# Kernel tuning notes

Hardware: AMD Instinct MI355X
Metric: run time of the kernel (lower is better)

The kernel has to match this reference:

```python
import jax, jax.numpy as jnp
import numpy as np

D_MODEL = 1024
D_STATE = 64
N_HEADS = 16
CHUNK = 64


def segsum(x):
    # x: (..., T) -> (..., T, T) with [i, j] = sum_{j<k<=i} x[k], -inf above diagonal
    T = x.shape[-1]
    xx = jnp.broadcast_to(x[..., None], x.shape + (T,))  # [i, j] = x[i]
    lower = jnp.tril(jnp.ones((T, T), dtype=bool), -1)
    xs = jnp.cumsum(jnp.where(lower, xx, 0.0), axis=-2)
    keep = jnp.tril(jnp.ones((T, T), dtype=bool), 0)
    return jnp.where(keep, xs, -jnp.inf)


def ssd_minimal(X, A, B, C, block_len):
    b, L, h, p = X.shape
    n = B.shape[-1]
    c = L // block_len
    l = block_len
    X = X.reshape(b, c, l, h, p)
    A = A.reshape(b, c, l, h).transpose(0, 3, 1, 2)  # b h c l
    B = B.reshape(b, c, l, h, n)
    C = C.reshape(b, c, l, h, n)
    A_cumsum = jnp.cumsum(A, axis=-1)  # b h c l
    Lmat = jnp.exp(segsum(A))  # b h c l l
    Y_diag = jnp.einsum('bclhn,bcshn,bhcls,bcshp->bclhp', C, B, Lmat, X)
    decay_states = jnp.exp(A_cumsum[:, :, :, -1:] - A_cumsum)  # b h c l
    states = jnp.einsum('bclhn,bhcl,bclhp->bchpn', B, decay_states, X)
    init = jnp.zeros_like(states[:, :1])
    states = jnp.concatenate([init, states], axis=1)  # b (c+1) h p n
    A_last = A_cumsum[:, :, :, -1]  # b h c
    decay_chunk = jnp.exp(segsum(jnp.pad(A_last, ((0, 0), (0, 0), (1, 0)))))  # b h (c+1) (c+1)
    new_states = jnp.einsum('bhzc,bchpn->bzhpn', decay_chunk, states)
    states, final_state = new_states[:, :-1], new_states[:, -1]
    state_decay_out = jnp.exp(A_cumsum)  # b h c l
    Y_off = jnp.einsum('bclhn,bchpn,bhcl->bclhp', C, states, state_decay_out)
    Y = (Y_diag + Y_off).reshape(b, L, h, p)
    return Y, final_state


def mamba2_forward(x, W_in, W_dt, b_dt, W_B, W_C, W_out, A_log):
    b, L, d = x.shape
    h, n = N_HEADS, D_STATE
    p = d // h
    # seqlen divisible by CHUNK -> no padding needed (pad_len == 0)
    xz = x @ W_in.T  # (b, L, 2d)
    x_in, z = xz[..., :d], xz[..., d:]
    dt = jax.nn.softplus(x @ W_dt.T + b_dt)  # (b, L, h)
    A = -jnp.exp(A_log)[None, None, :] * dt  # (b, L, h)
    B = (x @ W_B.T).reshape(b, L, h, n)
    C = (x @ W_C.T).reshape(b, L, h, n)
    X = x_in.reshape(b, L, h, p) * dt[..., None]
    Y, new_state = ssd_minimal(X, A, B, C, CHUNK)
    y = Y.reshape(b, L, d) * jax.nn.silu(z)
    y = y @ W_out.T
    return y, new_state


def setup_inputs() -> dict:
    key = jax.random.key(0)
    ks = jax.random.split(key, 7)
    d, h, n = D_MODEL, N_HEADS, D_STATE
    x = jax.random.normal(ks[0], (2, 4096, d), dtype=jnp.float32)
    # xavier_uniform with gain 0.5 for in/out proj
    lim_in = 0.5 * np.sqrt(6.0 / (d + 2 * d))
    W_in = jax.random.uniform(ks[1], (2 * d, d), minval=-lim_in, maxval=lim_in, dtype=jnp.float32)
    lim_out = 0.5 * np.sqrt(6.0 / (d + d))
    W_out = jax.random.uniform(ks[2], (d, d), minval=-lim_out, maxval=lim_out, dtype=jnp.float32)
    # default torch Linear init (kaiming-uniform-ish): U(-1/sqrt(fan_in), 1/sqrt(fan_in))
    lim = 1.0 / np.sqrt(d)
    W_dt = jax.random.uniform(ks[3], (h, d), minval=-lim, maxval=lim, dtype=jnp.float32)
    b_dt = jnp.zeros((h,), dtype=jnp.float32)
    W_B = jax.random.uniform(ks[4], (h * n, d), minval=-lim, maxval=lim, dtype=jnp.float32)
    W_C = jax.random.uniform(ks[5], (h * n, d), minval=-lim, maxval=lim, dtype=jnp.float32)
    A_log = jnp.log(jnp.linspace(1.0, 16.0, h)).astype(jnp.float32)
    return {"x": x, "W_in": W_in, "W_dt": W_dt, "b_dt": b_dt, "W_B": W_B, "W_C": W_C, "W_out": W_out, "A_log": A_log}


def reference(x, W_in, W_dt, b_dt, W_B, W_C, W_out, A_log):
    return mamba2_forward(x, W_in, W_dt, b_dt, W_B, W_C, W_out, A_log)
```

## Files before the change

### kernel.cpp

```cpp
#include <hip/hip_runtime.h>
#include <cstdint>
#include <cstddef>

#define NTOK 8192

typedef __bf16 bf16x8 __attribute__((ext_vector_type(8)));
typedef float f32x4 __attribute__((ext_vector_type(4)));
typedef float f32x4v __attribute__((ext_vector_type(4)));
typedef unsigned short u16x8 __attribute__((ext_vector_type(8)));

__device__ __forceinline__ float b2f(unsigned short u) {
    return __uint_as_float(((unsigned int)u) << 16);
}
__device__ __forceinline__ unsigned short f2b(float f) {
    unsigned int u = __float_as_uint(f);
    u += 0x7FFFu + ((u >> 16) & 1u);
    return (unsigned short)(u >> 16);
}

__device__ __forceinline__ void async_lds16(unsigned short* lds, const unsigned short* g) {
    __builtin_amdgcn_global_load_lds(
        (const __attribute__((address_space(1))) unsigned int*)g,
        (__attribute__((address_space(3))) unsigned int*)lds,
        16, 0, 0);
}

__global__ __launch_bounds__(256) void prep(
    const float* __restrict__ x, const float* __restrict__ W_in,
    const float* __restrict__ W_B, const float* __restrict__ W_C,
    unsigned short* __restrict__ xb, unsigned short* __restrict__ Wst,
    const float* __restrict__ s16a, const float* __restrict__ s16b,
    float* __restrict__ alogf, float* __restrict__ bdtf)
{
    const long i = (long)blockIdx.x * 256 + threadIdx.x;
    const float* src; unsigned short* dst; long off;
    if (i < 1048576)      { src = x;    dst = xb;            off = i; }
    else if (i < 1310720) { src = W_in; dst = Wst;           off = i - 1048576; }
    else if (i < 1441792) { src = W_B;  dst = Wst + 2097152; off = i - 1310720; }
    else if (i < 1572864) { src = W_C;  dst = Wst + 3145728; off = i - 1441792; }
    else {
        if (i == 1572864) {
            float ma = 0.f, mb = 0.f;
            for (int k = 0; k < 16; k++) { ma = fmaxf(ma, fabsf(s16a[k])); mb = fmaxf(mb, fabsf(s16b[k])); }
            const float* alog = (ma >= mb) ? s16a : s16b;
            const float* bdt  = (ma >= mb) ? s16b : s16a;
            for (int k = 0; k < 16; k++) { alogf[k] = alog[k]; bdtf[k] = bdt[k]; }
        }
        return;
    }
    const f32x4v* p = (const f32x4v*)(src + off * 8);
    f32x4v a = p[0], b = p[1];
    u16x8 v;
#pragma unroll
    for (int t = 0; t < 4; t++) { v[t] = f2b(a[t]); v[t + 4] = f2b(b[t]); }
    *(u16x8*)(dst + off * 8) = v;
}

__global__ __launch_bounds__(256) void f32_to_bf16(
    const float* __restrict__ in, unsigned short* __restrict__ out, int n8)
{
    const int i = blockIdx.x * 256 + threadIdx.x;
    if (i >= n8) return;
    const f32x4v* p = (const f32x4v*)(in + (long)i * 8);
    f32x4v a = p[0], b = p[1];
    u16x8 v;
#pragma unroll
    for (int t = 0; t < 4; t++) { v[t] = f2b(a[t]); v[t + 4] = f2b(b[t]); }
    *(u16x8*)(out + (long)i * 8) = v;
}

__global__ __launch_bounds__(256) void dt_kernel(
    const float* __restrict__ x, const float* __restrict__ Wdt,
    const float* __restrict__ bdt, const float* __restrict__ Alog,
    float* __restrict__ dtp, float* __restrict__ Ap)
{
    const int token = blockIdx.x * 16 + (threadIdx.x >> 4);
    const int h = threadIdx.x & 15;
    const f32x4v* xr = (const f32x4v*)(x + (long)token * 1024);
    const f32x4v* wr = (const f32x4v*)(Wdt + h * 1024);
    float s0 = bdt[h], s1 = 0.f;
#pragma unroll 8
    for (int k = 0; k < 256; k += 2) {
        f32x4v a0 = xr[k], w0 = wr[k];
        f32x4v a1 = xr[k + 1], w1 = wr[k + 1];
        s0 += a0[0] * w0[0] + a0[1] * w0[1] + a0[2] * w0[2] + a0[3] * w0[3];
        s1 += a1[0] * w1[0] + a1[1] * w1[1] + a1[2] * w1[2] + a1[3] * w1[3];
    }
    const float s = s0 + s1;
    const float dtv = (s > 15.f) ? s : log1pf(expf(s));
    dtp[token * 16 + h] = dtv;
    Ap[token * 16 + h] = -expf(Alog[h]) * dtv;
}

template <int MODE, int NI>
__global__ __launch_bounds__(512, 2) void gemm256(
    const unsigned short* __restrict__ A, const unsigned short* __restrict__ W,
    const int NT_N, const int N, const int K,
    void* __restrict__ out0, unsigned short* __restrict__ out1,
    unsigned short* __restrict__ out2, unsigned short* __restrict__ out3,
    const float* __restrict__ dtp)
{
    constexpr int BN = NI * 64;

    __shared__ unsigned short As[2][256 * 64];
    __shared__ unsigned short Ws[2][BN * 64];

    const int tid = threadIdx.x;
    const int lane = tid & 63;
    const int warp = tid >> 6;
    const int wm = warp >> 2;
    const int wn = warp & 3;
    const int qm = lane & 15;
    const int quad = lane >> 4;

    const int nwg = gridDim.x;
    const int cpx = nwg >> 3;
    const int bid = blockIdx.x;
    const int swz = (bid & 7) * cpx + (bid >> 3);
    const int bx = swz % NT_N;
    const int by = swz / NT_N;
    const long arow0 = (long)by * 256;
    const long wrow0 = (long)bx * BN;

    const int srow = tid >> 3;
    const int sgc = ((tid & 7) ^ (srow & 7)) * 8;

    f32x4 acc[8][NI];
    const f32x4 zero = {0.f, 0.f, 0.f, 0.f};
#pragma unroll
    for (int i = 0; i < 8; i++)
#pragma unroll
        for (int j = 0; j < NI; j++) acc[i][j] = zero;

    auto stage = [&](int buf, int k0) {
#pragma unroll
        for (int r = 0; r < 4; r++)
            async_lds16(As[buf] + r * 4096 + tid * 8,
                        A + (arow0 + r * 64 + srow) * (long)K + k0 + sgc);
#pragma unroll
        for (int r = 0; r < NI; r++)
            async_lds16(Ws[buf] + r * 4096 + tid * 8,
                        W + (wrow0 + r * 64 + srow) * (long)K + k0 + sgc);
    };
    const int rx = (qm & 7) << 3;
    auto compute = [&](const unsigned short* Ab, const unsigned short* Wb) {
#pragma unroll
        for (int kk = 0; kk < 64; kk += 32) {
            bf16x8 fa[8], fb[NI];
#pragma unroll
            for (int mi = 0; mi < 8; mi++) {
                const int row = wm * 128 + mi * 16 + qm;
                fa[mi] = *(const bf16x8*)(Ab + ((row * 64 + kk + quad * 8) ^ rx));
            }
#pragma unroll
            for (int ni = 0; ni < NI; ni++) {
                const int row = wn * (NI * 16) + ni * 16 + qm;
                fb[ni] = *(const bf16x8*)(Wb + ((row * 64 + kk + quad * 8) ^ rx));
            }
#pragma unroll
            for (int mi = 0; mi < 8; mi++)
#pragma unroll
                for (int ni = 0; ni < NI; ni++)
                    acc[mi][ni] = __builtin_amdgcn_mfma_f32_16x16x32_bf16(
                        fa[mi], fb[ni], acc[mi][ni], 0, 0, 0);
        }
    };

    const int nk = K >> 6;
    int cur = 0;
    stage(0, 0);
    __syncthreads();
    for (int t = 1; t < nk; t++) {
        stage(cur ^ 1, t << 6);
        compute(As[cur], Ws[cur]);
        __syncthreads();
        cur ^= 1;
    }
    compute(As[cur], Ws[cur]);

#pragma unroll
    for (int mi = 0; mi < 8; mi++)
#pragma unroll
        for (int ni = 0; ni < NI; ni++)
#pragma unroll
            for (int r = 0; r < 4; r++) {
                const long row = arow0 + wm * 128 + mi * 16 + quad * 4 + r;
                const int col = (int)wrow0 + wn * (NI * 16) + ni * 16 + qm;
                const float v = acc[mi][ni][r];
                if (MODE == 0) {
                    ((float*)out0)[row * N + col] = v;
                } else {
                    const int seg = col >> 10, cc = col & 1023;
                    if (seg == 0) {
                        ((unsigned short*)out0)[row * 1024 + cc] = f2b(v * dtp[row * 16 + (cc >> 6)]);
                    } else if (seg == 1) {
                        out1[row * 1024 + cc] = f2b(v / (1.f + expf(-v)));
                    } else if (seg == 2) {
                        out2[row * 1024 + cc] = f2b(v);
                    } else {
                        out3[row * 1024 + cc] = f2b(v);
                    }
                }
            }
}

__global__ __launch_bounds__(256) void ssd_states(
    const unsigned short* __restrict__ Xb, const unsigned short* __restrict__ Bb,
    const float* __restrict__ Ap, float* __restrict__ st_out,
    float* __restrict__ Alast)
{
    __shared__ __align__(16) unsigned short Xh[64 * 64];
    __shared__ __align__(16) unsigned short Xl[64 * 64];
    __shared__ __align__(16) unsigned short Bt[64 * 64];
    __shared__ float dec[64];

    const int blk = blockIdx.x;
    const int h = blk & 15;
    const int c = (blk >> 4) & 63;
    const int b = blk >> 10;
    const long tokenbase = (long)b * 4096 + (long)c * 64;
    const int tid = threadIdx.x;
    const int lane = tid & 63;
    const int w = tid >> 6;
    const int qm = lane & 15;
    const int quad = lane >> 4;

    const int row = tid & 63;
    u16x8 rx[2], rb[2];
#pragma unroll
    for (int i = 0; i < 2; i++) {
        const int ch = (tid >> 6) + 4 * i;
        const long g = (tokenbase + row) * 1024 + h * 64 + ch * 8;
        rx[i] = *(const u16x8*)(Xb + g);
        rb[i] = *(const u16x8*)(Bb + g);
    }
    if (tid < 64) {
        float v = Ap[(tokenbase + tid) * 16 + h];
#pragma unroll
        for (int off = 1; off < 64; off <<= 1) {
            const float u = __shfl_up(v, off, 64);
            if (tid >= off) v += u;
        }
        const float tot = __shfl(v, 63, 64);
        dec[tid] = expf(tot - v);
        if (tid == 63) Alast[(b * 16 + h) * 64 + c] = v;
    }
    __syncthreads();

    const float dv = dec[row];
#pragma unroll
    for (int i = 0; i < 2; i++) {
        const int ch = (tid >> 6) + 4 * i;
#pragma unroll
        for (int t = 0; t < 8; t++) {
            const int pn = ch * 8 + t;
            const int d = (pn * 64 + row) ^ (t << 3);
            const float xd = b2f(rx[i][t]) * dv;
            const unsigned short hi = f2b(xd);
            Xh[d] = hi;
            Xl[d] = f2b(xd - b2f(hi));
            Bt[d] = rb[i][t];
        }
    }
    __syncthreads();

    f32x4 acc[4];
    const f32x4 zero = {0.f, 0.f, 0.f, 0.f};
#pragma unroll
    for (int ni = 0; ni < 4; ni++) acc[ni] = zero;
#pragma unroll
    for (int kk2 = 0; kk2 < 2; kk2++) {
        const int ko = kk2 * 32 + quad * 8;
        const int ra = 16 * w + qm;
        const int da = (ra * 64 + ko) ^ ((ra & 7) << 3);
        bf16x8 fxh = *(const bf16x8*)(Xh + da);
        bf16x8 fxl = *(const bf16x8*)(Xl + da);
#pragma unroll
        for (int ni = 0; ni < 4; ni++) {
            const int rn = ni * 16 + qm;
            bf16x8 fb = *(const bf16x8*)(Bt + ((rn * 64 + ko) ^ ((rn & 7) << 3)));
            acc[ni] = __builtin_amdgcn_mfma_f32_16x16x32_bf16(fxh, fb, acc[ni], 0, 0, 0);
            acc[ni] = __builtin_amdgcn_mfma_f32_16x16x32_bf16(fxl, fb, acc[ni], 0, 0, 0);
        }
    }
    const long sbase = (long)blk * 4096;
    const int p0 = 16 * w + quad * 4;
#pragma unroll
    for (int ni = 0; ni < 4; ni++)
#pragma unroll
        for (int r = 0; r < 4; r++)
            st_out[sbase + (p0 + r) * 64 + ni * 16 + qm] = acc[ni][r];
}

__global__ __launch_bounds__(256) void scan_kernel(
    float* __restrict__ st, const float* __restrict__ Alast)
{
    __shared__ float eal[64];
    const int blk = blockIdx.x;
    const int grp = blk & 15;
    const int h = (blk >> 4) & 15;
    const int b = blk >> 8;
    const int e = grp * 256 + threadIdx.x;
    const float* al = Alast + (b * 16 + h) * 64;
    if (threadIdx.x < 64) eal[threadIdx.x] = expf(al[threadIdx.x]);
    __syncthreads();
    float M = 0.f;
    for (int c = 0; c < 64; c++) {
        const long idx = ((long)((b * 64 + c) * 16 + h)) * 4096 + e;
        const float s = st[idx];
        st[idx] = M;
        M = eal[c] * M + s;
    }
    st[(long)8388608 + (long)(b * 16 + h) * 4096 + e] = M;
}

__global__ __launch_bounds__(256) void ssd_yoff(
    const unsigned short* __restrict__ Xb, const unsigned short* __restrict__ Bb,
    const unsigned short* __restrict__ Cb, const float* __restrict__ Ap,
    const float* __restrict__ st, unsigned short* __restrict__ SZb)
{
    __shared__ __align__(16) unsigned short Bs[64 * 64];
    __shared__ __align__(16) unsigned short Ss[64 * 64];
    __shared__ __align__(16) unsigned short Xt[64 * 64];
    __shared__ __align__(16) unsigned short Gs[64 * 64];
    __shared__ float Acum[64];

    const int blk = blockIdx.x;
    const int h = blk & 15;
    const int c = (blk >> 4) & 63;
    const int b = blk >> 10;
    const long tokenbase = (long)b * 4096 + (long)c * 64;
    const int tid = threadIdx.x;
    const int lane = tid & 63;
    const int w = tid >> 6;
    const int qm = lane & 15;
    const int quad = lane >> 4;
    const long sbase = (long)blk * 4096;

    if (tid < 64) {
        float v = Ap[(tokenbase + tid) * 16 + h];
#pragma unroll
        for (int off = 1; off < 64; off <<= 1) {
            const float u = __shfl_up(v, off, 64);
            if (tid >= off) v += u;
        }
        Acum[tid] = v;
    }

#pragma unroll
    for (int i = 0; i < 2; i++) {
        const int idx = tid + i * 256;
        const int r8 = idx >> 3, c8 = (idx & 7) * 8;
        const long g = (tokenbase + r8) * 1024 + h * 64 + c8;
        const int d = (r8 * 64 + c8) ^ ((r8 & 7) << 3);
        *(u16x8*)(Bs + d) = *(const u16x8*)(Bb + g);
        const float* sp = st + sbase + r8 * 64 + c8;
        f32x4v s0 = *(const f32x4v*)sp, s1 = *(const f32x4v*)(sp + 4);
        u16x8 sv;
#pragma unroll
        for (int t = 0; t < 4; t++) { sv[t] = f2b(s0[t]); sv[t + 4] = f2b(s1[t]); }
        *(u16x8*)(Ss + d) = sv;
    }
    const int xrow = tid & 63;
#pragma unroll
    for (int i = 0; i < 2; i++) {
        const int ch = (tid >> 6) + 4 * i;
        const long g = (tokenbase + xrow) * 1024 + h * 64 + ch * 8;
        u16x8 xv = *(const u16x8*)(Xb + g);
#pragma unroll
        for (int t = 0; t < 8; t++) {
            const int p = ch * 8 + t;
            Xt[(p * 64 + xrow) ^ (t << 3)] = xv[t];
        }
    }
    u16x8 fc[2];
#pragma unroll
    for (int kk2 = 0; kk2 < 2; kk2++)
        fc[kk2] = *(const u16x8*)(Cb + (tokenbase + 16 * w + qm) * 1024 + h * 64 + kk2 * 32 + quad * 8);

    __syncthreads();

    f32x4 acc1[4], acc2[4];
    const f32x4 zero = {0.f, 0.f, 0.f, 0.f};
#pragma unroll
    for (int ni = 0; ni < 4; ni++) { acc1[ni] = zero; acc2[ni] = zero; }
#pragma unroll
    for (int kk2 = 0; kk2 < 2; kk2++) {
        const int ko = kk2 * 32 + quad * 8;
        bf16x8 fa = *(const bf16x8*)&fc[kk2];
#pragma unroll
        for (int ni = 0; ni < 4; ni++) {
            const int rn = ni * 16 + qm;
            const int d = (rn * 64 + ko) ^ ((rn & 7) << 3);
            bf16x8 fbb = *(const bf16x8*)(Bs + d);
            acc1[ni] = __builtin_amdgcn_mfma_f32_16x16x32_bf16(fa, fbb, acc1[ni], 0, 0, 0);
            bf16x8 fbs = *(const bf16x8*)(Ss + d);
            acc2[ni] = __builtin_amdgcn_mfma_f32_16x16x32_bf16(fa, fbs, acc2[ni], 0, 0, 0);
        }
    }

    const int l0 = 16 * w + quad * 4;
    float al[4];
#pragma unroll
    for (int r = 0; r < 4; r++) al[r] = Acum[l0 + r];
#pragma unroll
    for (int ni = 0; ni < 4; ni++) {
        const int s = ni * 16 + qm;
        const float as = Acum[s];
#pragma unroll
        for (int r = 0; r < 4; r++) {
            const int l = l0 + r;
            const float gv = (s <= l) ? acc1[ni][r] * expf(al[r] - as) : 0.f;
            Gs[(l * 64 + s) ^ ((l & 7) << 3)] = f2b(gv);
        }
    }
    __syncthreads();

    f32x4 acc3[4];
#pragma unroll
    for (int ni = 0; ni < 4; ni++) acc3[ni] = zero;
#pragma unroll
    for (int kk2 = 0; kk2 < 2; kk2++) {
        const int ko = kk2 * 32 + quad * 8;
        const int ra = 16 * w + qm;
        bf16x8 fg = *(const bf16x8*)(Gs + ((ra * 64 + ko) ^ ((ra & 7) << 3)));
#pragma unroll
        for (int ni = 0; ni < 4; ni++) {
            const int rp = ni * 16 + qm;
            bf16x8 fx = *(const bf16x8*)(Xt + ((rp * 64 + ko) ^ ((rp & 7) << 3)));
            acc3[ni] = __builtin_amdgcn_mfma_f32_16x16x32_bf16(fg, fx, acc3[ni], 0, 0, 0);
        }
    }
    float eds[4];
#pragma unroll
    for (int r = 0; r < 4; r++) eds[r] = expf(al[r]);
#pragma unroll
    for (int ni = 0; ni < 4; ni++) {
#pragma unroll
        for (int r = 0; r < 4; r++) {
            const int l = l0 + r;
            const int p = ni * 16 + qm;
            const float Y = acc3[ni][r] + eds[r] * acc2[ni][r];
            const long o = (tokenbase + l) * 1024 + h * 64 + p;
            SZb[o] = f2b(Y * b2f(SZb[o]));
        }
    }
}

extern "C" void kernel_launch(void* const* d_in, const int* in_sizes, int n_in,
                              void* d_out, int out_size, void* d_ws, size_t ws_size,
                              hipStream_t stream)
{
    int ix = 0, iwin = 1, iwdt = 2, i1m[3] = {4, 5, 6}, n1m = 0, i16[2] = {3, 7}, n16 = 0;
    for (int i = 0; i < n_in; i++) {
        switch (in_sizes[i]) {
            case 8388608: ix = i; break;
            case 2097152: iwin = i; break;
            case 16384:   iwdt = i; break;
            case 1048576: if (n1m < 3) i1m[n1m++] = i; break;
            case 16:      if (n16 < 2) i16[n16++] = i; break;
            default: break;
        }
    }
    if (n1m < 3) { i1m[0] = 4; i1m[1] = 5; i1m[2] = 6; }
    if (n16 < 2) { i16[0] = 3; i16[1] = 7; }
    const float* x     = (const float*)d_in[ix];
    const float* W_in  = (const float*)d_in[iwin];
    const float* W_dt  = (const float*)d_in[iwdt];
    const float* W_B   = (const float*)d_in[i1m[0]];
    const float* W_C   = (const float*)d_in[i1m[1]];
    const float* W_out = (const float*)d_in[i1m[2]];
    const float* s16a  = (const float*)d_in[i16[0]];
    const float* s16b  = (const float*)d_in[i16[1]];
    float* out = (float*)d_out;

    char* ws = (char*)d_ws;
    float* dtp   = (float*)(ws);
    float* Ap    = (float*)(ws + 524288);
    float* Alast = (float*)(ws + 1048576);
    float* Alogf = (float*)(ws + 1056768);
    float* bdtf  = (float*)(ws + 1056832);
    unsigned short* Xb  = (unsigned short*)(ws + 2097152);
    unsigned short* Bb  = (unsigned short*)(ws + 18874368);
    unsigned short* Cb  = (unsigned short*)(ws + 35651584);
    unsigned short* SZb = (unsigned short*)(ws + 52428800);

    unsigned short* xb  = (unsigned short*)d_out;
    unsigned short* Wst = (unsigned short*)((char*)d_out + 16777216);
    unsigned short* Wob = Xb;

    float* states = out;

    prep<<<6145, 256, 0, stream>>>(x, W_in, W_B, W_C, xb, Wst, s16a, s16b, Alogf, bdtf);
    dt_kernel<<<NTOK / 16, 256, 0, stream>>>(x, W_dt, bdtf, Alogf, dtp, Ap);
    gemm256<1, 4><<<512, 512, 0, stream>>>(xb, Wst, 16, 4096, 1024, Xb, SZb, Bb, Cb, dtp);
    ssd_states<<<2048, 256, 0, stream>>>(Xb, Bb, Ap, states, Alast);
    scan_kernel<<<512, 256, 0, stream>>>(states, Alast);
    ssd_yoff<<<2048, 256, 0, stream>>>(Xb, Bb, Cb, Ap, states, SZb);
    f32_to_bf16<<<512, 256, 0, stream>>>(W_out, Wob, 131072);
    gemm256<0, 2><<<256, 512, 0, stream>>>(SZb, Wob, 8, 1024, 1024, out, nullptr, nullptr, nullptr, nullptr);
}
```

Measured before the change: 366.7 us.

## Deepen GEMM prefetch to two stages with vmcnt waits; batch scan loads

```diff
diff --git a/kernel.cpp b/kernel.cpp
--- a/kernel.cpp
+++ b/kernel.cpp
@@ -23,6 +23,12 @@
         (const __attribute__((address_space(1))) unsigned int*)g,
         (__attribute__((address_space(3))) unsigned int*)lds,
         16, 0, 0);
+}
+
+template <int N> __device__ __forceinline__ void waitcnt_vm() {
+    if constexpr (N == 8)      asm volatile("s_waitcnt vmcnt(8)" ::: "memory");
+    else if constexpr (N == 6) asm volatile("s_waitcnt vmcnt(6)" ::: "memory");
+    else                       asm volatile("s_waitcnt vmcnt(0)" ::: "memory");
 }
 
 __global__ __launch_bounds__(256) void prep(
@@ -101,6 +107,7 @@
     const float* __restrict__ dtp)
 {
     constexpr int BN = NI * 64;
+    constexpr int LPS = 4 + NI;
 
     __shared__ unsigned short As[2][256 * 64];
     __shared__ unsigned short Ws[2][BN * 64];
@@ -167,16 +174,23 @@
     };
 
     const int nk = K >> 6;
-    int cur = 0;
     stage(0, 0);
-    __syncthreads();
-    for (int t = 1; t < nk; t++) {
-        stage(cur ^ 1, t << 6);
-        compute(As[cur], Ws[cur]);
-        __syncthreads();
-        cur ^= 1;
-    }
-    compute(As[cur], Ws[cur]);
+    stage(1, 64);
+    waitcnt_vm<LPS>();
+    __builtin_amdgcn_s_barrier();
+    for (int t = 0; t < nk; t++) {
+        compute(As[t & 1], Ws[t & 1]);
+        if (t + 1 < nk) {
+            __builtin_amdgcn_s_barrier();
+            if (t + 2 < nk) {
+                stage(t & 1, (t + 2) << 6);
+                waitcnt_vm<LPS>();
+            } else {
+                waitcnt_vm<0>();
+            }
+            __builtin_amdgcn_s_barrier();
+        }
+    }
 
 #pragma unroll
     for (int mi = 0; mi < 8; mi++)
@@ -304,12 +318,19 @@
     const float* al = Alast + (b * 16 + h) * 64;
     if (threadIdx.x < 64) eal[threadIdx.x] = expf(al[threadIdx.x]);
     __syncthreads();
+    const long base = ((long)(b * 64 * 16 + h)) * 4096 + e;
+    const long cstep = (long)16 * 4096;
     float M = 0.f;
-    for (int c = 0; c < 64; c++) {
-        const long idx = ((long)((b * 64 + c) * 16 + h)) * 4096 + e;
-        const float s = st[idx];
-        st[idx] = M;
-        M = eal[c] * M + s;
+    for (int c = 0; c < 64; c += 4) {
+        const long i0 = base + (long)c * cstep;
+        const float s0 = st[i0];
+        const float s1 = st[i0 + cstep];
+        const float s2 = st[i0 + 2 * cstep];
+        const float s3 = st[i0 + 3 * cstep];
+        st[i0] = M;              M = eal[c] * M + s0;
+        st[i0 + cstep] = M;      M = eal[c + 1] * M + s1;
+        st[i0 + 2 * cstep] = M;  M = eal[c + 2] * M + s2;
+        st[i0 + 3 * cstep] = M;  M = eal[c + 3] * M + s3;
     }
     st[(long)8388608 + (long)(b * 16 + h) * 4096 + e] = M;
 }
```

New measurement: 357.3 us. -2.6%, faster.
